# Kernel tuning notes

Measured on AMD Instinct MI355X. Metric: run time of the kernel, lower is better.

## Reference

```python
import jax, jax.numpy as jnp
import numpy as np


def _interp_linear(c, out_len):
    """PyTorch F.interpolate(mode='linear', align_corners=False) along last axis.
    c: (d, in_len) -> (d, out_len). Half-pixel coordinate mapping."""
    in_len = c.shape[-1]
    scale = in_len / out_len
    src = (jnp.arange(out_len, dtype=jnp.float32) + 0.5) * scale - 0.5
    src = jnp.clip(src, 0.0, in_len - 1)
    lo = jnp.floor(src).astype(jnp.int32)
    hi = jnp.minimum(lo + 1, in_len - 1)
    w = (src - lo.astype(jnp.float32)).astype(c.dtype)
    return c[..., lo] * (1.0 - w) + c[..., hi] * w


def _causal_spectrum(spec, fft_size):
    """Given the real part of a causal kernel's spectrum (1, F, d) with
    F = fft_size//2+1, recover the full complex spectrum via the Hilbert
    transform (analytic-signal window in time domain)."""
    t = jnp.fft.irfft(spec, n=fft_size, axis=1)  # even real kernel (1, fft_size, d)
    w = jnp.ones((fft_size,), dtype=t.dtype)
    w = w.at[1:fft_size // 2].set(2.0)
    w = w.at[fft_size // 2 + 1:].set(0.0)
    return jnp.fft.rfft(t * w[None, :, None], axis=1)  # (1, F, d) complex


def setup_inputs() -> dict:
    key = jax.random.key(0)
    k1, k2 = jax.random.split(key)
    B, N, D, NUM_FREQS = 8, 8192, 512, 512
    x = jax.random.normal(k1, (B, N, D), dtype=jnp.float32)
    coeffs = jax.random.normal(k2, (D, NUM_FREQS), dtype=jnp.float32)
    dc = jnp.ones((D, 1), dtype=jnp.float32)
    return {"x": x, "coeffs": coeffs, "dc": dc}


def reference(x, coeffs, dc):
    n = x.shape[-2]
    fft_size = int(2 ** int(np.ceil(np.log2(2 * n))))
    # interpolate learned real frequency coefficients up to fft_size//2 bins
    pos = _interp_linear(coeffs, fft_size // 2)          # (d, fft_size//2)
    a = jnp.concatenate([dc, pos], axis=1)               # (d, fft_size//2+1)
    a = jnp.transpose(a)[None]                           # (1, F, d)
    spec = _causal_spectrum(a, fft_size)                 # (1, F, d) complex
    xf = jnp.fft.rfft(x, n=fft_size, axis=-2)            # (B, F, d)
    out = jnp.fft.irfft(xf * spec, n=fft_size, axis=-2)  # (B, fft_size, d)
    return out[..., :n, :]
```

## Files before the change

kernel.cpp:

```cpp
#include <hip/hip_runtime.h>


typedef float v2f __attribute__((ext_vector_type(2)));

#define PQ_STRIDE 4097
constexpr double PI_D = 3.14159265358979323846;

__device__ v2f    g_twA[15][512];
__device__ v2f    g_twB[15][32];
__device__ v2f    g_w81[4096];
__device__ v2f    g_h[4096];
__device__ float4 g_u[4097];

__device__ __forceinline__ v2f mkv2(float x, float y) { v2f r; r.x = x; r.y = y; return r; }
__device__ __forceinline__ v2f cmul(v2f a, v2f b)  { return mkv2(a.x, a.x) * b + mkv2(-a.y, a.y) * b.yx; }
__device__ __forceinline__ v2f cmulc(v2f a, v2f b) { return mkv2(a.x, -a.x) * b + mkv2(a.y, a.y) * b.yx; }
__device__ __forceinline__ v2f cmulcA(v2f a, v2f b){ return mkv2(a.x, a.x) * b + mkv2(a.y, -a.y) * b.yx; }

#define SLOT(k) ((((k) & 3) << 2) | ((k) >> 2))

__device__ __forceinline__ int addr1(int n2, int k1) {
    return (n2 << 4) | ((k1 + n2) & 15);
}
__device__ __forceinline__ int addr2(int r, int m2) {
    return (r << 5) | ((m2 + 2 * r) & 31);
}
__device__ __forceinline__ int addr3(int k) {
    int lo = (k + 2 * (k >> 4) + (k >> 8) + (k >> 12)) & 15;
    return (k & ~15) | lo;
}

template <int SGN>
__device__ __forceinline__ void fft4(v2f& a, v2f& b, v2f& c, v2f& d) {
    v2f A0 = a + c, A1 = a - c, A2 = b + d, A3 = b - d;
    v2f T = (SGN < 0) ? mkv2(A3.y, -A3.x) : mkv2(-A3.y, A3.x);
    a = A0 + A2; b = A1 + T; c = A0 - A2; d = A1 - T;
}

template <int SGN>
__device__ __forceinline__ void fft16_tail(v2f* v) {
    const float C1 = 0.9238795325112867f, S1 = 0.3826834323650898f, R2 = 0.7071067811865476f;
    v[5]  = cmul(v[5],  mkv2(C1, SGN < 0 ? -S1 : S1));
    v[6]  = cmul(v[6],  mkv2(R2, SGN < 0 ? -R2 : R2));
    v[7]  = cmul(v[7],  mkv2(S1, SGN < 0 ? -C1 : C1));
    v[9]  = cmul(v[9],  mkv2(R2, SGN < 0 ? -R2 : R2));
    v[10] = (SGN < 0) ? mkv2(v[10].y, -v[10].x) : mkv2(-v[10].y, v[10].x);
    v[11] = cmul(v[11], mkv2(-R2, SGN < 0 ? -R2 : R2));
    v[13] = cmul(v[13], mkv2(S1, SGN < 0 ? -C1 : C1));
    v[14] = cmul(v[14], mkv2(-R2, SGN < 0 ? -R2 : R2));
    v[15] = cmul(v[15], mkv2(-C1, SGN < 0 ? S1 : -S1));
    fft4<SGN>(v[0], v[1], v[2], v[3]);
    fft4<SGN>(v[4], v[5], v[6], v[7]);
    fft4<SGN>(v[8], v[9], v[10], v[11]);
    fft4<SGN>(v[12], v[13], v[14], v[15]);
}
template <int SGN>
__device__ __forceinline__ void fft16(v2f* v) {
    fft4<SGN>(v[0], v[4], v[8], v[12]);
    fft4<SGN>(v[1], v[5], v[9], v[13]);
    fft4<SGN>(v[2], v[6], v[10], v[14]);
    fft4<SGN>(v[3], v[7], v[11], v[15]);
    fft16_tail<SGN>(v);
}
template <int SGN>
__device__ __forceinline__ void fft16_half(v2f* v) {
    #pragma unroll
    for (int j = 0; j < 4; ++j) {
        v2f a = v[j], b = v[j + 4];
        v2f T = (SGN < 0) ? mkv2(b.y, -b.x) : mkv2(-b.y, b.x);
        v[j] = a + b; v[j + 4] = a + T;
        v[j + 8] = a - b; v[j + 12] = a - T;
    }
    fft16_tail<SGN>(v);
}

__device__ __forceinline__ v2f shflx1(v2f v) {
    return mkv2(__shfl_xor(v.x, 1), __shfl_xor(v.y, 1));
}

#define W32_TABLES \
    constexpr float WC[16] = {1.f, 0.98078528f, 0.92387953f, 0.83146961f, 0.70710678f, \
        0.55557023f, 0.38268343f, 0.19509032f, 0.f, -0.19509032f, -0.38268343f, \
        -0.55557023f, -0.70710678f, -0.83146961f, -0.92387953f, -0.98078528f}; \
    constexpr float WS[16] = {0.f, 0.19509032f, 0.38268343f, 0.55557023f, 0.70710678f, \
        0.83146961f, 0.92387953f, 0.98078528f, 1.f, 0.98078528f, 0.92387953f, \
        0.83146961f, 0.70710678f, 0.55557023f, 0.38268343f, 0.19509032f};

__device__ __forceinline__ void fwd_L2_L3(v2f* sbuf, int tid) {
    {
        int k1 = tid >> 5, m2 = tid & 31;
        v2f w[15];
        #pragma unroll
        for (int j = 0; j < 15; ++j) w[j] = g_twB[j][m2];
        v2f u[16];
        #pragma unroll
        for (int m1 = 0; m1 < 16; ++m1) u[m1] = sbuf[addr1(32 * m1 + m2, k1)];
        __syncthreads();
        fft16<-1>(u);
        #pragma unroll
        for (int k = 1; k < 16; ++k) u[SLOT(k)] = cmul(u[SLOT(k)], w[k - 1]);
        #pragma unroll
        for (int q1 = 0; q1 < 16; ++q1) sbuf[addr2(k1 * 16 + q1, m2)] = u[SLOT(q1)];
        __syncthreads();
    }
    {
        int k1 = tid >> 5, q1 = (tid >> 1) & 15, half = tid & 1;
        v2f e[16];
        #pragma unroll
        for (int j = 0; j < 16; ++j) e[j] = sbuf[addr2(k1 * 16 + q1, 2 * j + half)];
        __syncthreads();
        fft16<-1>(e);
        W32_TABLES
        #pragma unroll
        for (int q = 0; q < 16; ++q) {
            v2f mine = e[SLOT(q)];
            v2f othr = shflx1(mine);
            v2f Eq = half ? othr : mine;
            v2f Oq = half ? mine : othr;
            v2f WO = cmul(mkv2(WC[q], -WS[q]), Oq);
            v2f X = half ? Eq - WO : Eq + WO;
            int k = k1 + 16 * q1 + 256 * (q + 16 * half);
            sbuf[addr3(k)] = X;
        }
        __syncthreads();
    }
}

__device__ __forceinline__ void inv_L3_L2(v2f* sbuf, int tid) {
    {
        int k1 = tid >> 5, q1 = (tid >> 1) & 15, half = tid & 1;
        v2f t[16];
        #pragma unroll
        for (int q = 0; q < 16; ++q)
            t[q] = sbuf[addr3(k1 + 16 * q1 + 256 * (q + 16 * half))];
        __syncthreads();
        W32_TABLES
        #pragma unroll
        for (int q = 0; q < 16; ++q) {
            v2f othr = shflx1(t[q]);
            if (half) t[q] = cmul(mkv2(WC[q], WS[q]), othr - t[q]);
            else      t[q] = t[q] + othr;
        }
        fft16<1>(t);
        #pragma unroll
        for (int j = 0; j < 16; ++j) sbuf[addr2(k1 * 16 + q1, 2 * j + half)] = t[SLOT(j)];
        __syncthreads();
    }
    {
        int k1 = tid >> 5, m2 = tid & 31;
        v2f w[15];
        #pragma unroll
        for (int j = 0; j < 15; ++j) w[j] = g_twB[j][m2];
        v2f u[16];
        #pragma unroll
        for (int q1 = 0; q1 < 16; ++q1) u[q1] = sbuf[addr2(k1 * 16 + q1, m2)];
        __syncthreads();
        #pragma unroll
        for (int k = 1; k < 16; ++k) u[k] = cmulc(u[k], w[k - 1]);
        fft16<1>(u);
        #pragma unroll
        for (int m1 = 0; m1 < 16; ++m1) sbuf[addr1(32 * m1 + m2, k1)] = u[SLOT(m1)];
        __syncthreads();
    }
}

__device__ __forceinline__ void inv_L1(const v2f* sbuf, int tid, v2f* v) {
    v2f w[15];
    #pragma unroll
    for (int j = 0; j < 15; ++j) w[j] = g_twA[j][tid];
    #pragma unroll
    for (int k1 = 0; k1 < 16; ++k1) v[k1] = sbuf[addr1(tid, k1)];
    #pragma unroll
    for (int k = 1; k < 16; ++k) v[k] = cmulc(v[k], w[k - 1]);
    fft16<1>(v);
}

__device__ __forceinline__ float aval(const float* C, float dcv, int idx) {
    if (idx == 0) return dcv;
    int j = idx - 1;
    float src = ((float)j + 0.5f) * 0.0625f - 0.5f;
    src = fminf(fmaxf(src, 0.0f), 511.0f);
    int lo = (int)floorf(src);
    int hi = min(lo + 1, 511);
    float w = src - (float)lo;
    return C[lo] * (1.0f - w) + C[hi] * w;
}

__device__ __forceinline__ void spec_single(v2f* sbuf, const float4* PQd, int k) {
    float4 uu = g_u[k];
    float4 pq = PQd[k];
    v2f P = mkv2(pq.x, pq.y), Q = mkv2(pq.z, pq.w);
    v2f al = P + Q;
    v2f R  = P * uu.x - Q * uu.y;
    int a = addr3(k);
    v2f Z = sbuf[a];
    v2f W = cmulc(R, Z);
    sbuf[a] = cmul(al, Z) + mkv2(-W.y, W.x);
}
__device__ __forceinline__ void spec_pair(v2f* sbuf, const float4* PQd, int k) {
    int m = 8192 - k;
    float4 uu = g_u[k];
    float4 pq = PQd[k];
    v2f P = mkv2(pq.x, pq.y), Q = mkv2(pq.z, pq.w);
    int ak = addr3(k), am = addr3(m);
    v2f Zk = sbuf[ak], Zm = sbuf[am];
    v2f al = P + Q;
    v2f R  = P * uu.x - Q * uu.y;
    v2f Dt = P * uu.z + Q * uu.w;
    v2f W = cmulc(R, Zm);
    v2f V = cmul(R, Zk);
    sbuf[ak] = cmul(al, Zk) + mkv2(-W.y, W.x);
    sbuf[am] = cmulcA(Dt, Zm) + V.yx;
}

__global__ void k_init() {
    int t = blockIdx.x * 512 + threadIdx.x;
    if (t < 4096) {
        double th = (PI_D / 8192.0) * (double)t;
        double s = sin(th), c = cos(th);
        g_w81[t] = mkv2((float)c, (float)s);
        g_h[t]   = mkv2((float)(0.5 * (1.0 - s)), (float)(0.5 * (1.0 + s)));
    }
    if (t <= 4096) {
        if (t == 4096) {
            g_u[t] = make_float4(0.f, 0.f, 0.f, 0.f);
        } else {
            double th = (PI_D / 8192.0) * (double)t;
            double s = sin(th), c = cos(th);
            g_u[t] = make_float4((float)(c / (1.0 - s)), (float)(c / (1.0 + s)),
                                 (float)((1.0 + s) / (1.0 - s)), (float)((1.0 - s) / (1.0 + s)));
        }
    }
    if (t < 7680) {
        int j = t >> 9, tt = t & 511;
        double th = -(PI_D / 4096.0) * (double)(tt * (j + 1));
        g_twA[j][tt] = mkv2((float)cos(th), (float)sin(th));
    }
    if (t < 480) {
        int j = t >> 5, m2 = t & 31;
        double th = -(PI_D / 256.0) * (double)(m2 * (j + 1));
        g_twB[j][m2] = mkv2((float)cos(th), (float)sin(th));
    }
}

__global__ __launch_bounds__(512, 4) void k01(const float* __restrict__ x,
                                              const float* __restrict__ coeffs,
                                              const float* __restrict__ dc,
                                              float4* __restrict__ PQ,
                                              v2f* __restrict__ zin) {
    __shared__ v2f sbuf[8192];
    int tid = threadIdx.x;
    if (blockIdx.x < 512) {
        int d = blockIdx.x;
        const float* C = coeffs + d * 512;
        float dcv = dc[d];
        #pragma unroll
        for (int tt = 0; tt < 16; ++tt) {
            int k = tid + (tt << 9);
            float ak = aval(C, dcv, k);
            float am = aval(C, dcv, 8192 - k);
            float Ae = 0.5f * (ak + am), Ao = 0.5f * (ak - am);
            float sn, cs;
            if (tt < 8) { v2f w = g_w81[k];        cs = w.x;  sn = w.y; }
            else        { v2f w = g_w81[k - 4096]; cs = -w.y; sn = w.x; }
            sbuf[addr3(k)] = mkv2(Ae - Ao * sn, Ao * cs);
        }
        __syncthreads();
        inv_L3_L2(sbuf, tid);
        v2f v[16];
        inv_L1(sbuf, tid, v);
        v2f u[16];
        #pragma unroll
        for (int n1 = 0; n1 < 16; ++n1) {
            v2f z = v[SLOT(n1)];
            int n = (n1 << 9) + tid;
            float te = z.x * (1.0f / 8192.0f);
            float to = z.y * (1.0f / 8192.0f);
            int m0 = 2 * n;
            float he = (m0 == 0) ? te : ((m0 < 8192) ? 2.0f * te : ((m0 == 8192) ? te : 0.0f));
            float ho = (m0 + 1 < 8192) ? 2.0f * to : 0.0f;
            u[n1] = mkv2(he, ho);
        }
        fft16<-1>(u);
        v2f wA[15];
        #pragma unroll
        for (int j = 0; j < 15; ++j) wA[j] = g_twA[j][tid];
        #pragma unroll
        for (int k = 1; k < 16; ++k) u[SLOT(k)] = cmul(u[SLOT(k)], wA[k - 1]);
        #pragma unroll
        for (int k1 = 0; k1 < 16; ++k1) sbuf[addr1(tid, k1)] = u[SLOT(k1)];
        __syncthreads();
        fwd_L2_L3(sbuf, tid);
        float4* PQd = PQ + (size_t)d * PQ_STRIDE;
        const float scale = 1.0f / 8192.0f;
        #pragma unroll
        for (int tt = 0; tt < 8; ++tt) {
            int k = tid + (tt << 9);
            if (k == 0) {
                v2f Z0 = sbuf[addr3(0)];
                float S0 = (Z0.x + Z0.y) * scale;
                float SM = (Z0.x - Z0.y) * scale;
                PQd[0] = make_float4(0.5f * S0, 0.0f, 0.5f * SM, 0.0f);
                v2f Z4 = sbuf[addr3(4096)];
                float px = 0.5f * Z4.x * scale, py = 0.5f * Z4.y * scale;
                PQd[4096] = make_float4(px, py, px, py);
            } else {
                int km = 8192 - k;
                v2f Zk = sbuf[addr3(k)], Zm = sbuf[addr3(km)];
                v2f Xe = mkv2((Zk.x + Zm.x) * 0.5f, (Zk.y - Zm.y) * 0.5f);
                v2f dz = mkv2((Zk.x - Zm.x) * 0.5f, (Zk.y + Zm.y) * 0.5f);
                v2f Xo = mkv2(dz.y, -dz.x);
                v2f w = g_w81[k];
                v2f wXo = cmulc(Xo, w);
                v2f Sk  = (Xe + wXo) * scale;
                v2f SmC = (Xe - wXo) * scale;
                v2f h = g_h[k];
                v2f Pk = Sk * h.x, Qk = SmC * h.y;
                PQd[k] = make_float4(Pk.x, Pk.y, Qk.x, Qk.y);
            }
        }
    } else {
        int bid = blockIdx.x - 512;
        int nt = bid & 127, dt = (bid >> 7) & 7, bb = bid >> 10;
        float* tile = (float*)sbuf;
        const float4* x4 = (const float4*)(x + ((size_t)bb * 8192 + (size_t)nt * 64) * 512 + dt * 64);
        int lane4 = tid & 15, row = tid >> 4;
        #pragma unroll
        for (int r = 0; r < 2; ++r) {
            int rr = row + 32 * r;
            float4 vv = x4[(size_t)rr * 128 + lane4];
            float* dst = &tile[rr * 65 + lane4 * 4];
            dst[0] = vv.x; dst[1] = vv.y; dst[2] = vv.z; dst[3] = vv.w;
        }
        __syncthreads();
        int tx4 = tid & 15, dl = tid >> 4;
        #pragma unroll
        for (int r = 0; r < 2; ++r) {
            int dloc = dl + 32 * r;
            int d = dt * 64 + dloc;
            int npb = nt * 32 + 2 * tx4;
            float4 w;
            w.x = tile[(4 * tx4 + 0) * 65 + dloc];
            w.y = tile[(4 * tx4 + 1) * 65 + dloc];
            w.z = tile[(4 * tx4 + 2) * 65 + dloc];
            w.w = tile[(4 * tx4 + 3) * 65 + dloc];
            *(float4*)&zin[((size_t)(d * 8 + bb)) * 4096 + npb] = w;
        }
    }
}

__global__ __launch_bounds__(512, 4) void k2_conv(const v2f* __restrict__ zin,
                                                  const float4* __restrict__ PQ,
                                                  v2f* __restrict__ yout) {
    __shared__ v2f sbuf[8192];
    int wg = blockIdx.x, tid = threadIdx.x;
    int xcd = wg & 7, idx = wg >> 3;
    int d = (xcd << 6) | (idx >> 3), b = idx & 7;
    int io = d * 8 + b;
    const v2f* zi = zin + (size_t)io * 4096;
    const float4* PQd = PQ + (size_t)d * PQ_STRIDE;
    v2f v[16];
    #pragma unroll
    for (int n1 = 0; n1 < 8; ++n1) v[n1] = zi[(n1 << 9) + tid];
    v2f wA[15];
    #pragma unroll
    for (int j = 0; j < 15; ++j) wA[j] = g_twA[j][tid];
    fft16_half<-1>(v);
    #pragma unroll
    for (int k = 1; k < 16; ++k) v[SLOT(k)] = cmul(v[SLOT(k)], wA[k - 1]);
    #pragma unroll
    for (int k1 = 0; k1 < 16; ++k1) sbuf[addr1(tid, k1)] = v[SLOT(k1)];
    __syncthreads();
    fwd_L2_L3(sbuf, tid);
    #pragma unroll
    for (int tt = 0; tt < 8; ++tt) {
        int k = tid + (tt << 9);
        if (k == 0) { spec_single(sbuf, PQd, 0); spec_single(sbuf, PQd, 4096); }
        else        { spec_pair(sbuf, PQd, k); }
    }
    __syncthreads();
    inv_L3_L2(sbuf, tid);
    inv_L1(sbuf, tid, v);
    v2f* yo = yout + (size_t)io * 4096;
    #pragma unroll
    for (int n1 = 0; n1 < 8; ++n1) yo[(n1 << 9) + tid] = v[SLOT(n1)];
}

__global__ __launch_bounds__(512) void k3_unpack(const float2* __restrict__ yout,
                                                 float* __restrict__ out) {
    __shared__ float2 tile[64 * 33];
    int bid = blockIdx.x;
    int nt = bid & 127, dt = (bid >> 7) & 7, bb = bid >> 10;
    int tid = threadIdx.x;
    const float4* y4 = (const float4*)yout;
    int tx4 = tid & 15, dl = tid >> 4;
    #pragma unroll
    for (int r = 0; r < 2; ++r) {
        int dloc = dl + 32 * r;
        int d = dt * 64 + dloc;
        float4 vv = y4[(size_t)(d * 8 + bb) * 2048 + nt * 16 + tx4];
        tile[dloc * 33 + 2 * tx4]     = make_float2(vv.x, vv.y);
        tile[dloc * 33 + 2 * tx4 + 1] = make_float2(vv.z, vv.w);
    }
    __syncthreads();
    const float* tf = (const float*)tile;
    int lane4 = tid & 15, nl = tid >> 4;
    #pragma unroll
    for (int r = 0; r < 2; ++r) {
        int nloc = nl + 32 * r;
        int npl = nloc >> 1, e = nloc & 1;
        float4 w;
        w.x = tf[((4 * lane4 + 0) * 33 + npl) * 2 + e];
        w.y = tf[((4 * lane4 + 1) * 33 + npl) * 2 + e];
        w.z = tf[((4 * lane4 + 2) * 33 + npl) * 2 + e];
        w.w = tf[((4 * lane4 + 3) * 33 + npl) * 2 + e];
        int n = nt * 64 + nloc;
        *(float4*)&out[((size_t)bb * 8192 + n) * 512 + dt * 64 + lane4 * 4] = w;
    }
}

extern "C" void kernel_launch(void* const* d_in, const int* in_sizes, int n_in,
                              void* d_out, int out_size, void* d_ws, size_t ws_size,
                              hipStream_t stream) {
    const float* x      = (const float*)d_in[0];
    const float* coeffs = (const float*)d_in[1];
    const float* dc     = (const float*)d_in[2];
    float* out = (float*)d_out;

    float4* PQ  = (float4*)d_ws;
    v2f*    zbuf = (v2f*)((char*)d_ws + (size_t)512 * PQ_STRIDE * sizeof(float4));

    k_init<<<15, 512, 0, stream>>>();
    k01<<<512 + 8192, 512, 0, stream>>>(x, coeffs, dc, PQ, zbuf);
    k2_conv<<<4096, 512, 0, stream>>>(zbuf, PQ, zbuf);
    k3_unpack<<<8192, 512, 0, stream>>>((const float2*)zbuf, out);
}
```

Baseline: 487.8 us.

## Split 8192-point convolution FFT into even/odd 4096-point halves

The conv kernel now handles the zero-padded 8192-point FFT as two 4096-point transforms: one on the even bins, and one on the odd bins after pre-twiddling the input. Each half runs forward FFT, spectral multiply and inverse FFT in 4096 entries of shared memory with 256 threads. The two halves are then combined with a twiddle on output. This halves LDS use per block and the block size, which should raise occupancy. In exchange the kernel reads the input twice, does extra twiddle multiplies, and gives up the half-zero shortcut in the first radix stage.

```diff
diff --git a/kernel.cpp b/kernel.cpp
--- a/kernel.cpp
+++ b/kernel.cpp
@@ -11,6 +11,9 @@
 __device__ v2f    g_w81[4096];
 __device__ v2f    g_h[4096];
 __device__ float4 g_u[4097];
+__device__ v2f    g_tA4[15][256];
+__device__ v2f    g_tB4[15][16];
+__device__ v2f    g_wt4[256];
 
 __device__ __forceinline__ v2f mkv2(float x, float y) { v2f r; r.x = x; r.y = y; return r; }
 __device__ __forceinline__ v2f cmul(v2f a, v2f b)  { return mkv2(a.x, a.x) * b + mkv2(-a.y, a.y) * b.yx; }
@@ -28,6 +31,16 @@
 __device__ __forceinline__ int addr3(int k) {
     int lo = (k + 2 * (k >> 4) + (k >> 8) + (k >> 12)) & 15;
     return (k & ~15) | lo;
+}
+
+__device__ __forceinline__ int addrA4(int t, int k1) {
+    return (t << 4) | ((k1 + t) & 15);
+}
+__device__ __forceinline__ int addrB4(int r, int n3) {
+    return (r << 4) | ((n3 + r) & 15);
+}
+__device__ __forceinline__ int addrX4(int k) {
+    return (k & ~15) | ((k + (k >> 4) + 2 * (k >> 8)) & 15);
 }
 
 template <int SGN>
@@ -86,6 +99,7 @@
         0.83146961f, 0.92387953f, 0.98078528f, 1.f, 0.98078528f, 0.92387953f, \
         0.83146961f, 0.70710678f, 0.55557023f, 0.38268343f, 0.19509032f};
 
+
 __device__ __forceinline__ void fwd_L2_L3(v2f* sbuf, int tid) {
     {
         int k1 = tid >> 5, m2 = tid & 31;
@@ -186,23 +200,22 @@
     return C[lo] * (1.0f - w) + C[hi] * w;
 }
 
-__device__ __forceinline__ void spec_single(v2f* sbuf, const float4* PQd, int k) {
-    float4 uu = g_u[k];
-    float4 pq = PQd[k];
+__device__ __forceinline__ void spec_single4(v2f* sbuf, const float4* PQd, int j, int korig) {
+    float4 uu = g_u[korig];
+    float4 pq = PQd[korig];
     v2f P = mkv2(pq.x, pq.y), Q = mkv2(pq.z, pq.w);
     v2f al = P + Q;
     v2f R  = P * uu.x - Q * uu.y;
-    int a = addr3(k);
+    int a = addrX4(j);
     v2f Z = sbuf[a];
     v2f W = cmulc(R, Z);
     sbuf[a] = cmul(al, Z) + mkv2(-W.y, W.x);
 }
-__device__ __forceinline__ void spec_pair(v2f* sbuf, const float4* PQd, int k) {
-    int m = 8192 - k;
-    float4 uu = g_u[k];
-    float4 pq = PQd[k];
+__device__ __forceinline__ void spec_pair4(v2f* sbuf, const float4* PQd, int j, int jm, int korig) {
+    float4 uu = g_u[korig];
+    float4 pq = PQd[korig];
     v2f P = mkv2(pq.x, pq.y), Q = mkv2(pq.z, pq.w);
-    int ak = addr3(k), am = addr3(m);
+    int ak = addrX4(j), am = addrX4(jm);
     v2f Zk = sbuf[ak], Zm = sbuf[am];
     v2f al = P + Q;
     v2f R  = P * uu.x - Q * uu.y;
@@ -213,6 +226,93 @@
     sbuf[am] = cmulcA(Dt, Zm) + V.yx;
 }
 
+template <int PARITY>
+__device__ __forceinline__ void conv4096(v2f* sbuf, int tid, v2f* v, const float4* PQd) {
+    int k1 = tid >> 4, lo = tid & 15;
+    fft16<-1>(v);
+    {
+        v2f w[15];
+        #pragma unroll
+        for (int j = 0; j < 15; ++j) w[j] = g_tA4[j][tid];
+        #pragma unroll
+        for (int k = 1; k < 16; ++k) v[SLOT(k)] = cmul(v[SLOT(k)], w[k - 1]);
+    }
+    #pragma unroll
+    for (int q = 0; q < 16; ++q) sbuf[addrA4(tid, q)] = v[SLOT(q)];
+    __syncthreads();
+    {
+        v2f u[16];
+        #pragma unroll
+        for (int n2 = 0; n2 < 16; ++n2) u[n2] = sbuf[addrA4(n2 * 16 + lo, k1)];
+        __syncthreads();
+        fft16<-1>(u);
+        v2f w[15];
+        #pragma unroll
+        for (int j = 0; j < 15; ++j) w[j] = g_tB4[j][lo];
+        #pragma unroll
+        for (int k = 1; k < 16; ++k) u[SLOT(k)] = cmul(u[SLOT(k)], w[k - 1]);
+        #pragma unroll
+        for (int k2 = 0; k2 < 16; ++k2) sbuf[addrB4(k1 * 16 + k2, lo)] = u[SLOT(k2)];
+        __syncthreads();
+    }
+    {
+        v2f e[16];
+        #pragma unroll
+        for (int n3 = 0; n3 < 16; ++n3) e[n3] = sbuf[addrB4(k1 * 16 + lo, n3)];
+        __syncthreads();
+        fft16<-1>(e);
+        #pragma unroll
+        for (int k3 = 0; k3 < 16; ++k3) sbuf[addrX4(k1 + 16 * lo + 256 * k3)] = e[SLOT(k3)];
+        __syncthreads();
+    }
+    #pragma unroll
+    for (int t = 0; t < 8; ++t) {
+        int j = tid + (t << 8);
+        if (PARITY == 0) {
+            if (j == 0) { spec_single4(sbuf, PQd, 0, 0); spec_single4(sbuf, PQd, 2048, 4096); }
+            else        spec_pair4(sbuf, PQd, j, 4096 - j, 2 * j);
+        } else {
+            spec_pair4(sbuf, PQd, j, 4095 - j, 2 * j + 1);
+        }
+    }
+    __syncthreads();
+    {
+        v2f t[16];
+        #pragma unroll
+        for (int k3 = 0; k3 < 16; ++k3) t[k3] = sbuf[addrX4(k1 + 16 * lo + 256 * k3)];
+        __syncthreads();
+        fft16<1>(t);
+        #pragma unroll
+        for (int n3 = 0; n3 < 16; ++n3) sbuf[addrB4(k1 * 16 + lo, n3)] = t[SLOT(n3)];
+        __syncthreads();
+    }
+    {
+        v2f u[16];
+        #pragma unroll
+        for (int k2 = 0; k2 < 16; ++k2) u[k2] = sbuf[addrB4(k1 * 16 + k2, lo)];
+        __syncthreads();
+        v2f w[15];
+        #pragma unroll
+        for (int j = 0; j < 15; ++j) w[j] = g_tB4[j][lo];
+        #pragma unroll
+        for (int k = 1; k < 16; ++k) u[k] = cmulc(u[k], w[k - 1]);
+        fft16<1>(u);
+        #pragma unroll
+        for (int n2 = 0; n2 < 16; ++n2) sbuf[addrA4(n2 * 16 + lo, k1)] = u[SLOT(n2)];
+        __syncthreads();
+    }
+    {
+        #pragma unroll
+        for (int q = 0; q < 16; ++q) v[q] = sbuf[addrA4(tid, q)];
+        v2f w[15];
+        #pragma unroll
+        for (int j = 0; j < 15; ++j) w[j] = g_tA4[j][tid];
+        #pragma unroll
+        for (int k = 1; k < 16; ++k) v[k] = cmulc(v[k], w[k - 1]);
+        fft16<1>(v);
+    }
+}
+
 __global__ void k_init() {
     int t = blockIdx.x * 512 + threadIdx.x;
     if (t < 4096) {
@@ -240,6 +340,20 @@
         int j = t >> 5, m2 = t & 31;
         double th = -(PI_D / 256.0) * (double)(m2 * (j + 1));
         g_twB[j][m2] = mkv2((float)cos(th), (float)sin(th));
+    }
+    if (t < 3840) {
+        int j = t >> 8, tt = t & 255;
+        double th = -(2.0 * PI_D / 4096.0) * (double)(tt * (j + 1));
+        g_tA4[j][tt] = mkv2((float)cos(th), (float)sin(th));
+    }
+    if (t < 240) {
+        int j = t >> 4, n3 = t & 15;
+        double th = -(2.0 * PI_D / 256.0) * (double)(n3 * (j + 1));
+        g_tB4[j][n3] = mkv2((float)cos(th), (float)sin(th));
+    }
+    if (t < 256) {
+        double th = -(2.0 * PI_D / 8192.0) * (double)t;
+        g_wt4[t] = mkv2((float)cos(th), (float)sin(th));
     }
 }
 
@@ -349,41 +463,41 @@
     }
 }
 
-__global__ __launch_bounds__(512, 4) void k2_conv(const v2f* __restrict__ zin,
+__global__ __launch_bounds__(256, 5) void k2_conv(const v2f* __restrict__ zin,
                                                   const float4* __restrict__ PQ,
                                                   v2f* __restrict__ yout) {
-    __shared__ v2f sbuf[8192];
+    __shared__ v2f sbuf[4096];
     int wg = blockIdx.x, tid = threadIdx.x;
     int xcd = wg & 7, idx = wg >> 3;
     int d = (xcd << 6) | (idx >> 3), b = idx & 7;
     int io = d * 8 + b;
     const v2f* zi = zin + (size_t)io * 4096;
     const float4* PQd = PQ + (size_t)d * PQ_STRIDE;
+    W32_TABLES
+
     v2f v[16];
     #pragma unroll
-    for (int n1 = 0; n1 < 8; ++n1) v[n1] = zi[(n1 << 9) + tid];
-    v2f wA[15];
-    #pragma unroll
-    for (int j = 0; j < 15; ++j) wA[j] = g_twA[j][tid];
-    fft16_half<-1>(v);
-    #pragma unroll
-    for (int k = 1; k < 16; ++k) v[SLOT(k)] = cmul(v[SLOT(k)], wA[k - 1]);
-    #pragma unroll
-    for (int k1 = 0; k1 < 16; ++k1) sbuf[addr1(tid, k1)] = v[SLOT(k1)];
+    for (int n1 = 0; n1 < 16; ++n1) v[n1] = zi[(n1 << 8) + tid];
+    conv4096<0>(sbuf, tid, v, PQd);
+    v2f ye[16];
+    #pragma unroll
+    for (int i = 0; i < 16; ++i) ye[i] = v[i];
     __syncthreads();
-    fwd_L2_L3(sbuf, tid);
-    #pragma unroll
-    for (int tt = 0; tt < 8; ++tt) {
-        int k = tid + (tt << 9);
-        if (k == 0) { spec_single(sbuf, PQd, 0); spec_single(sbuf, PQd, 4096); }
-        else        { spec_pair(sbuf, PQd, k); }
-    }
-    __syncthreads();
-    inv_L3_L2(sbuf, tid);
-    inv_L1(sbuf, tid, v);
+
+    v2f wt = g_wt4[tid];
+    #pragma unroll
+    for (int n1 = 0; n1 < 16; ++n1) {
+        v2f t16 = cmul(wt, mkv2(WC[n1], -WS[n1]));
+        v[n1] = cmul(zi[(n1 << 8) + tid], t16);
+    }
+    conv4096<1>(sbuf, tid, v, PQd);
+
     v2f* yo = yout + (size_t)io * 4096;
     #pragma unroll
-    for (int n1 = 0; n1 < 8; ++n1) yo[(n1 << 9) + tid] = v[SLOT(n1)];
+    for (int n1 = 0; n1 < 16; ++n1) {
+        v2f t16 = cmul(wt, mkv2(WC[n1], -WS[n1]));
+        yo[(n1 << 8) + tid] = ye[SLOT(n1)] + cmulc(v[SLOT(n1)], t16);
+    }
 }
 
 __global__ __launch_bounds__(512) void k3_unpack(const float2* __restrict__ yout,
@@ -432,6 +546,6 @@
 
     k_init<<<15, 512, 0, stream>>>();
     k01<<<512 + 8192, 512, 0, stream>>>(x, coeffs, dc, PQ, zbuf);
-    k2_conv<<<4096, 512, 0, stream>>>(zbuf, PQ, zbuf);
+    k2_conv<<<4096, 256, 0, stream>>>(zbuf, PQ, zbuf);
     k3_unpack<<<8192, 512, 0, stream>>>((const float2*)zbuf, out);
 }
```

New measurement: 926.6 us. 1.9x slower.
